# Optimization experiments

Hardware: AMD Instinct MI355X
Metric: run time of the kernel (lower is better)

## Reference

```python
import jax, jax.numpy as jnp
import numpy as np

B_SZ, SEQ, H = 8, 1024, 2048
LN_EPS = 1e-6
CLIP = 1.0e6


def setup_inputs() -> dict:
    key = jax.random.key(0)
    ks = jax.random.split(key, 8)
    lecun = 1.0 / np.sqrt(H)
    return {
        "x": jax.random.normal(ks[0], (B_SZ, SEQ, H), dtype=jnp.float32),
        "context": jnp.zeros((B_SZ, H), dtype=jnp.float32),
        # learned params
        "A": -jax.random.uniform(ks[1], (H,), dtype=jnp.float32),  # diagonal decay (zeros-init in src; small negative for stable decay)
        "Bm": jax.random.normal(ks[2], (H, H), dtype=jnp.float32) * lecun,
        "Cm": jax.random.normal(ks[3], (H, H), dtype=jnp.float32) * lecun,
        "dt_kernel": jax.random.normal(ks[4], (H, 1), dtype=jnp.float32) * 0.02,
        "dt_bias": jnp.zeros((1,), dtype=jnp.float32),
        "gate_kernel": jax.random.normal(ks[5], (H, H), dtype=jnp.float32) * lecun,
        "gate_bias": jnp.zeros((H,), dtype=jnp.float32),
        "ln_scale": jnp.ones((H,), dtype=jnp.float32),
        "ln_bias": jnp.zeros((H,), dtype=jnp.float32),
    }


def _layernorm(x, scale, bias):
    mu = jnp.mean(x, axis=-1, keepdims=True)
    var = jnp.mean(jnp.square(x - mu), axis=-1, keepdims=True)
    return (x - mu) * jax.lax.rsqrt(var + LN_EPS) * scale + bias


def reference(x, context, A, Bm, Cm, dt_kernel, dt_bias, gate_kernel, gate_bias, ln_scale, ln_bias):
    xn = jnp.clip(_layernorm(x, ln_scale, ln_bias), -CLIP, CLIP)  # [B,S,H]
    xt = jnp.swapaxes(xn, 0, 1)  # time-major [S,B,H]

    def step(state, x_t):
        # x_t: [B,H]; delta: [B,1] from Dense(1)
        delta = jnp.exp(x_t @ dt_kernel + dt_bias)
        decay = jnp.exp(delta * A)                  # [B,H] via broadcast
        new_state = state * decay + x_t @ Bm        # [B,H]
        out = new_state @ Cm                        # [B,H]
        return new_state, out

    final_state, ys = jax.lax.scan(step, context, xt)
    outputs = jnp.swapaxes(ys, 0, 1)  # [B,S,H]
    gate = outputs @ gate_kernel + gate_bias
    outputs = outputs * jax.nn.sigmoid(gate)  # GLU
    # dropout deterministic (training=False) -> identity
    return outputs, final_state
```

## Files before the change

kernel.cpp:

```cpp
#include <hip/hip_runtime.h>
#include <hip/hip_bf16.h>

#define H_DIM 2048
#define B_SZ  8
#define SEQ   1024
#define M_DIM (B_SZ*SEQ)
#define KDIM  2048
#define NKT   (KDIM/64)
#define CCH   32
#define CLEN  (SEQ/CCH)

using f32x4 = __attribute__((ext_vector_type(4))) float;
using s16x8 = __attribute__((ext_vector_type(8))) short;

__device__ __forceinline__ float bf2f(unsigned short u) {
  unsigned int x = ((unsigned int)u) << 16;
  return __builtin_bit_cast(float, x);
}
__device__ __forceinline__ unsigned short f2bf(float f) {
  unsigned int x = __builtin_bit_cast(unsigned int, f);
  unsigned int r = (x + 0x7fffu + ((x >> 16) & 1u)) >> 16;
  return (unsigned short)r;
}

__device__ __forceinline__ void gl_lds16(const void* g, void* l) {
  __builtin_amdgcn_global_load_lds(
      (__attribute__((address_space(1))) void*)g,
      (__attribute__((address_space(3))) void*)l, 16, 0, 0);
}

__global__ __launch_bounds__(256) void transpose3_kernel(
    const float* __restrict__ s0, unsigned short* __restrict__ d0,
    const float* __restrict__ s1, unsigned short* __restrict__ d1,
    const float* __restrict__ s2, unsigned short* __restrict__ d2)
{
  const float* src = (blockIdx.z == 0) ? s0 : (blockIdx.z == 1) ? s1 : s2;
  unsigned short* dst = (blockIdx.z == 0) ? d0 : (blockIdx.z == 1) ? d1 : d2;
  __shared__ float t[32][33];
  int tx = threadIdx.x & 31, ty = threadIdx.x >> 5;
  int c0 = blockIdx.x << 5, r0 = blockIdx.y << 5;
#pragma unroll
  for (int i = 0; i < 32; i += 8)
    t[ty + i][tx] = src[(size_t)(r0 + ty + i) * H_DIM + (c0 + tx)];
  __syncthreads();
#pragma unroll
  for (int i = 0; i < 32; i += 8)
    dst[(size_t)(c0 + ty + i) * H_DIM + (r0 + tx)] = f2bf(t[tx][ty + i]);
}

__global__ __launch_bounds__(256) void ln_delta_kernel(
    const float* __restrict__ x, const float* __restrict__ lns,
    const float* __restrict__ lnb, const float* __restrict__ dtk,
    const float* __restrict__ dtb, unsigned short* __restrict__ xn,
    float* __restrict__ delta)
{
  const int row = blockIdx.x;
  const int tid = threadIdx.x;
  const float* xr = x + (size_t)row * H_DIM;
  float v[8];
  *(float4*)&v[0] = ((const float4*)xr)[tid * 2];
  *(float4*)&v[4] = ((const float4*)xr)[tid * 2 + 1];
  float s1 = 0.f, s2 = 0.f;
#pragma unroll
  for (int j = 0; j < 8; ++j) { s1 += v[j]; s2 += v[j] * v[j]; }
  __shared__ float red[8];
#pragma unroll
  for (int off = 32; off; off >>= 1) {
    s1 += __shfl_down(s1, off);
    s2 += __shfl_down(s2, off);
  }
  if ((tid & 63) == 0) { red[tid >> 6] = s1; red[4 + (tid >> 6)] = s2; }
  __syncthreads();
  float mean = (red[0] + red[1] + red[2] + red[3]) * (1.0f / H_DIM);
  float var  = (red[4] + red[5] + red[6] + red[7]) * (1.0f / H_DIM) - mean * mean;
  float rstd = rsqrtf(var + 1e-6f);

  float sc[8], bi[8], dk[8];
  *(float4*)&sc[0] = ((const float4*)lns)[tid * 2];
  *(float4*)&sc[4] = ((const float4*)lns)[tid * 2 + 1];
  *(float4*)&bi[0] = ((const float4*)lnb)[tid * 2];
  *(float4*)&bi[4] = ((const float4*)lnb)[tid * 2 + 1];
  *(float4*)&dk[0] = ((const float4*)dtk)[tid * 2];
  *(float4*)&dk[4] = ((const float4*)dtk)[tid * 2 + 1];

  float dot = 0.f;
  s16x8 o;
#pragma unroll
  for (int j = 0; j < 8; ++j) {
    float xv = (v[j] - mean) * rstd * sc[j] + bi[j];
    xv = fminf(fmaxf(xv, -1.0e6f), 1.0e6f);
    dot += xv * dk[j];
    o[j] = (short)f2bf(xv);
  }
  *(s16x8*)(xn + (size_t)row * H_DIM + tid * 8) = o;

  __syncthreads();
#pragma unroll
  for (int off = 32; off; off >>= 1) dot += __shfl_down(dot, off);
  if ((tid & 63) == 0) red[tid >> 6] = dot;
  __syncthreads();
  if (tid == 0)
    delta[row] = __expf(red[0] + red[1] + red[2] + red[3] + dtb[0]);
}

__global__ __launch_bounds__(256) void scan1_kernel(
    const unsigned short* __restrict__ U, const float* __restrict__ delta,
    const float* __restrict__ Adiag, float* __restrict__ Q, float* __restrict__ P)
{
  const int h = blockIdx.x * 1024 + threadIdx.x * 4;
  const int c = blockIdx.y, b = blockIdx.z;
  const float4 a = *(const float4*)(Adiag + h);
  const unsigned short* u = U + ((size_t)b * SEQ + c * CLEN) * H_DIM + h;
  const float* dl = delta + b * SEQ + c * CLEN;
  float4 st = {0.f, 0.f, 0.f, 0.f};
  float4 pr = {1.f, 1.f, 1.f, 1.f};
#pragma unroll 8
  for (int s = 0; s < CLEN; ++s) {
    const float d = dl[s];
    const ushort4 uv = *(const ushort4*)(u + (size_t)s * H_DIM);
    const float dx = __expf(d * a.x), dy = __expf(d * a.y);
    const float dz = __expf(d * a.z), dw = __expf(d * a.w);
    st.x = fmaf(st.x, dx, bf2f(uv.x)); st.y = fmaf(st.y, dy, bf2f(uv.y));
    st.z = fmaf(st.z, dz, bf2f(uv.z)); st.w = fmaf(st.w, dw, bf2f(uv.w));
    pr.x *= dx; pr.y *= dy; pr.z *= dz; pr.w *= dw;
  }
  const size_t idx = ((size_t)b * CCH + c) * H_DIM + h;
  *(float4*)(Q + idx) = st;
  *(float4*)(P + idx) = pr;
}

__global__ __launch_bounds__(256) void scan2_kernel(
    const float* __restrict__ Q, const float* __restrict__ P,
    const float* __restrict__ ctx, float* __restrict__ sIn,
    float* __restrict__ finalSt)
{
  const int h = blockIdx.x * 256 + threadIdx.x;
  const int b = blockIdx.y;
  float s = ctx[b * H_DIM + h];
#pragma unroll
  for (int c = 0; c < CCH; ++c) {
    const size_t idx = ((size_t)b * CCH + c) * H_DIM + h;
    sIn[idx] = s;
    s = fmaf(s, P[idx], Q[idx]);
  }
  finalSt[b * H_DIM + h] = s;
}

__global__ __launch_bounds__(256) void scan3_kernel(
    const unsigned short* __restrict__ U, const float* __restrict__ delta,
    const float* __restrict__ Adiag, const float* __restrict__ sIn,
    unsigned short* __restrict__ states)
{
  const int h = blockIdx.x * 1024 + threadIdx.x * 4;
  const int c = blockIdx.y, b = blockIdx.z;
  const float4 a = *(const float4*)(Adiag + h);
  const unsigned short* u = U + ((size_t)b * SEQ + c * CLEN) * H_DIM + h;
  unsigned short* so = states + ((size_t)b * SEQ + c * CLEN) * H_DIM + h;
  const float* dl = delta + b * SEQ + c * CLEN;
  float4 st = *(const float4*)(sIn + ((size_t)b * CCH + c) * H_DIM + h);
#pragma unroll 8
  for (int s = 0; s < CLEN; ++s) {
    const float d = dl[s];
    const ushort4 uv = *(const ushort4*)(u + (size_t)s * H_DIM);
    const float dx = __expf(d * a.x), dy = __expf(d * a.y);
    const float dz = __expf(d * a.z), dw = __expf(d * a.w);
    st.x = fmaf(st.x, dx, bf2f(uv.x)); st.y = fmaf(st.y, dy, bf2f(uv.y));
    st.z = fmaf(st.z, dz, bf2f(uv.z)); st.w = fmaf(st.w, dw, bf2f(uv.w));
    ushort4 ov = { f2bf(st.x), f2bf(st.y), f2bf(st.z), f2bf(st.w) };
    *(ushort4*)(so + (size_t)s * H_DIM) = ov;
  }
}


#define BARR()  __builtin_amdgcn_s_barrier();
#define LGKM0() asm volatile("s_waitcnt lgkmcnt(0)");
#define VMC(N)  asm volatile("s_waitcnt vmcnt(" #N ")" ::: "memory");

#define RD_A(DST, PL, PHH, OFF) { _Pragma("unroll") for (int i_ = 0; i_ < 4; ++i_) { \
    DST[0][i_] = *(const s16x8*)((PL) + (OFF) + i_ * 4096); \
    DST[1][i_] = *(const s16x8*)((PHH) + (OFF) + i_ * 4096); } }
#define RD_B(DST, PL, PHH, OFF) { _Pragma("unroll") for (int j_ = 0; j_ < 2; ++j_) { \
    DST[0][j_] = *(const s16x8*)((PL) + (OFF) + j_ * 8192); \
    DST[1][j_] = *(const s16x8*)((PHH) + (OFF) + j_ * 8192); } }

#define QMM(IB, JB, AF, BF) { __builtin_amdgcn_s_setprio(1); \
  _Pragma("unroll") for (int i_ = 0; i_ < 4; ++i_) \
  _Pragma("unroll") for (int j_ = 0; j_ < 2; ++j_) { \
    acc[(IB)+i_][(JB)+j_] = __builtin_amdgcn_mfma_f32_16x16x32_bf16(AF[0][i_], BF[0][j_], acc[(IB)+i_][(JB)+j_], 0, 0, 0); \
    acc[(IB)+i_][(JB)+j_] = __builtin_amdgcn_mfma_f32_16x16x32_bf16(AF[1][i_], BF[1][j_], acc[(IB)+i_][(JB)+j_], 0, 0, 0); } \
  __builtin_amdgcn_s_setprio(0); }

#define STAGE_A(BUF, HH, TT) { const char* s_ = srcA + (HH) * 524288 + (TT) * 128; \
  char* d_ = ldsA + (BUF) * 32768 + (HH) * 16384 + tid16; \
  gl_lds16(s_, d_); gl_lds16(s_ + 262144, d_ + 8192); }
#define STAGE_B(BUF, HH, TT) { const char* s_ = srcB + (HH) * 524288 + (TT) * 128; \
  char* d_ = ldsB + (BUF) * 32768 + (HH) * 16384 + tid16; \
  gl_lds16(s_, d_); gl_lds16(s_ + 262144, d_ + 8192); }

template <int EPI>
__global__ __launch_bounds__(512, 2) void gemm8p(
    const char* __restrict__ Ab, const char* __restrict__ Bb,
    float* __restrict__ outF, unsigned short* __restrict__ outH,
    const unsigned short* __restrict__ Ybf, const float* __restrict__ gbias)
{
  extern __shared__ char lds[];
  char* ldsA = lds;
  char* ldsB = lds + 65536;

  const int tid  = threadIdx.x;
  const int lane = tid & 63, wid = tid >> 6;
  const int wr = wid >> 2, wc = wid & 3;
  const int fr = lane & 15, kq = lane >> 4;

  const int bid = blockIdx.x;
  const int xcd = bid & 7;
  const int li  = bid >> 3;
  const int bm  = (xcd >> 1) * 8 + (li & 7);
  const int bn  = (xcd & 1) * 4 + (li >> 3);

  const int grow = tid >> 3;
  const int gswz = ((tid & 7) ^ (grow & 7)) << 4;
  const char* srcA = Ab + ((size_t)(bm * 256 + grow)) * 4096 + gswz;
  const char* srcB = Bb + ((size_t)(bn * 256 + grow)) * 4096 + gswz;
  const int tid16 = tid << 4;

  const int sw0 = ((kq ^ (fr & 7)) << 4);
  const int sw1 = (((4 | kq) ^ (fr & 7)) << 4);
  const char* pa0b0 = ldsA + wr * 2048 + fr * 128 + sw0;
  const char* pa1b0 = ldsA + wr * 2048 + fr * 128 + sw1;
  const char* pa0b1 = pa0b0 + 32768;
  const char* pa1b1 = pa1b0 + 32768;
  const char* pb0b0 = ldsB + wc * 2048 + fr * 128 + sw0;
  const char* pb1b0 = ldsB + wc * 2048 + fr * 128 + sw1;
  const char* pb0b1 = pb0b0 + 32768;
  const char* pb1b1 = pb1b0 + 32768;

  f32x4 acc[8][4] = {};
  s16x8 a03[2][4], a47[2][4], b01[2][2], b23[2][2];

  STAGE_A(0, 0, 0); STAGE_B(0, 0, 0); STAGE_B(0, 1, 0); STAGE_A(0, 1, 0);
  VMC(4);
  STAGE_A(1, 0, 1); STAGE_B(1, 0, 1); STAGE_B(1, 1, 1);
  VMC(6);
  BARR();

  for (int t = 0; t < NKT / 2 - 1; ++t) {
    const int T0 = 2 * t;
    RD_A(a03, pa0b0, pa1b0, 0);
    RD_B(b01, pb0b0, pb1b0, 0);
    STAGE_A(1, 1, T0 + 1);
    BARR(); LGKM0(); QMM(0, 0, a03, b01); BARR();
    RD_B(b23, pb0b0, pb1b0, 16384);
    STAGE_A(0, 0, T0 + 2);
    BARR(); LGKM0(); QMM(0, 2, a03, b23); BARR();
    RD_A(a47, pa0b0, pa1b0, 16384);
    STAGE_B(0, 0, T0 + 2);
    BARR(); LGKM0(); QMM(4, 0, a47, b01); BARR();
    STAGE_B(0, 1, T0 + 2);
    BARR(); QMM(4, 2, a47, b23); VMC(6); BARR();
    RD_A(a03, pa0b1, pa1b1, 0);
    RD_B(b01, pb0b1, pb1b1, 0);
    STAGE_A(0, 1, T0 + 2);
    BARR(); LGKM0(); QMM(0, 0, a03, b01); BARR();
    RD_B(b23, pb0b1, pb1b1, 16384);
    STAGE_A(1, 0, T0 + 3);
    BARR(); LGKM0(); QMM(0, 2, a03, b23); BARR();
    RD_A(a47, pa0b1, pa1b1, 16384);
    STAGE_B(1, 0, T0 + 3);
    BARR(); LGKM0(); QMM(4, 0, a47, b01); BARR();
    STAGE_B(1, 1, T0 + 3);
    BARR(); QMM(4, 2, a47, b23); VMC(6); BARR();
  }

  RD_A(a03, pa0b0, pa1b0, 0);
  RD_B(b01, pb0b0, pb1b0, 0);
  STAGE_A(1, 1, 31);
  BARR(); LGKM0(); QMM(0, 0, a03, b01); BARR();
  RD_B(b23, pb0b0, pb1b0, 16384);
  BARR(); LGKM0(); QMM(0, 2, a03, b23); BARR();
  RD_A(a47, pa0b0, pa1b0, 16384);
  BARR(); LGKM0(); QMM(4, 0, a47, b01); BARR();
  BARR(); QMM(4, 2, a47, b23); VMC(0); BARR();
  RD_A(a03, pa0b1, pa1b1, 0);
  RD_B(b01, pb0b1, pb1b1, 0);
  QMM(0, 0, a03, b01);
  RD_B(b23, pb0b1, pb1b1, 16384);
  QMM(0, 2, a03, b23);
  RD_A(a47, pa0b1, pa1b1, 16384);
  QMM(4, 0, a47, b01);
  QMM(4, 2, a47, b23);

  __syncthreads();
  const int cr = (lane >> 4) << 2;
  const int cc = lane & 15;
  if constexpr (EPI == 1) {
#pragma unroll
    for (int i = 0; i < 8; ++i)
#pragma unroll
      for (int j = 0; j < 4; ++j)
#pragma unroll
        for (int r = 0; r < 4; ++r) {
          const int row = (2 * i + wr) * 16 + cr + r;
          const int col = (4 * j + wc) * 16 + cc;
          const int off = (row * 512 + col * 2) ^ ((row & 7) << 4);
          *(unsigned short*)(lds + off) = f2bf(acc[i][j][r]);
        }
    __syncthreads();
#pragma unroll
    for (int it = 0; it < 16; ++it) {
      const int L = it * 8192 + tid * 16;
      const int row = L >> 9, inrow = L & 511;
      const s16x8 v = *(const s16x8*)(lds + (L ^ ((row & 7) << 4)));
      *(s16x8*)(outH + ((size_t)(bm * 256 + row)) * H_DIM + bn * 256 + (inrow >> 1)) = v;
    }
  } else {
#pragma unroll
    for (int p = 0; p < 2; ++p) {
      if (p) __syncthreads();
#pragma unroll
      for (int i = 4 * p; i < 4 * p + 4; ++i)
#pragma unroll
        for (int j = 0; j < 4; ++j)
#pragma unroll
          for (int r = 0; r < 4; ++r) {
            const int lrow = (2 * i + wr) * 16 + cr + r - 128 * p;
            const int col = (4 * j + wc) * 16 + cc;
            const int off = (lrow * 1024 + col * 4) ^ ((lrow & 7) << 4);
            *(float*)(lds + off) = acc[i][j][r];
          }
      __syncthreads();
#pragma unroll
      for (int it = 0; it < 16; ++it) {
        const int L = it * 8192 + tid * 16;
        const int lrow = L >> 10, inrow = L & 1023;
        const f32x4 v = *(const f32x4*)(lds + (L ^ ((lrow & 7) << 4)));
        const size_t growg = (size_t)(bm * 256 + 128 * p + lrow);
        const int gcol = bn * 256 + (inrow >> 2);
        const float4 gb4 = *(const float4*)(gbias + gcol);
        const ushort4 y4 = *(const ushort4*)(Ybf + growg * H_DIM + gcol);
        float4 o;
        o.x = bf2f(y4.x) / (1.f + __expf(-(v[0] + gb4.x)));
        o.y = bf2f(y4.y) / (1.f + __expf(-(v[1] + gb4.y)));
        o.z = bf2f(y4.z) / (1.f + __expf(-(v[2] + gb4.z)));
        o.w = bf2f(y4.w) / (1.f + __expf(-(v[3] + gb4.w)));
        *(float4*)(outF + growg * H_DIM + gcol) = o;
      }
    }
  }
}

extern "C" void kernel_launch(void* const* d_in, const int* in_sizes, int n_in,
                              void* d_out, int out_size, void* d_ws, size_t ws_size,
                              hipStream_t stream) {
  (void)in_sizes; (void)n_in; (void)out_size; (void)ws_size;
  const float* x     = (const float*)d_in[0];
  const float* ctx   = (const float*)d_in[1];
  const float* Adiag = (const float*)d_in[2];
  const float* Bm    = (const float*)d_in[3];
  const float* Cm    = (const float*)d_in[4];
  const float* dtk   = (const float*)d_in[5];
  const float* dtb   = (const float*)d_in[6];
  const float* gk    = (const float*)d_in[7];
  const float* gb    = (const float*)d_in[8];
  const float* lns   = (const float*)d_in[9];
  const float* lnb   = (const float*)d_in[10];
  float* outF = (float*)d_out;

  char* ws = (char*)d_ws;
  unsigned short* xnY    = (unsigned short*)ws; ws += (size_t)M_DIM * H_DIM * 2;
  unsigned short* U      = (unsigned short*)ws; ws += (size_t)M_DIM * H_DIM * 2;
  unsigned short* states = (unsigned short*)ws; ws += (size_t)M_DIM * H_DIM * 2;
  unsigned short* T1     = (unsigned short*)ws; ws += (size_t)H_DIM * H_DIM * 2;
  unsigned short* T2     = (unsigned short*)ws; ws += (size_t)H_DIM * H_DIM * 2;
  unsigned short* T3     = (unsigned short*)ws; ws += (size_t)H_DIM * H_DIM * 2;
  float* delta           = (float*)ws;          ws += (size_t)M_DIM * 4;
  float* Qbuf            = (float*)ws;          ws += (size_t)B_SZ * CCH * H_DIM * 4;
  float* Pbuf            = (float*)ws;          ws += (size_t)B_SZ * CCH * H_DIM * 4;
  float* sInBuf          = (float*)ws;          ws += (size_t)B_SZ * CCH * H_DIM * 4;

  hipFuncSetAttribute((const void*)&gemm8p<1>,
                      hipFuncAttributeMaxDynamicSharedMemorySize, 131072);
  hipFuncSetAttribute((const void*)&gemm8p<2>,
                      hipFuncAttributeMaxDynamicSharedMemorySize, 131072);

  dim3 tb(256);
  transpose3_kernel<<<dim3(64, 64, 3), tb, 0, stream>>>(Bm, T1, Cm, T2, gk, T3);
  ln_delta_kernel<<<M_DIM, tb, 0, stream>>>(x, lns, lnb, dtk, dtb, xnY, delta);
  gemm8p<1><<<256, 512, 131072, stream>>>(
      (const char*)xnY, (const char*)T1, nullptr, U, nullptr, nullptr);
  scan1_kernel<<<dim3(H_DIM / 1024, CCH, B_SZ), tb, 0, stream>>>(
      U, delta, Adiag, Qbuf, Pbuf);
  scan2_kernel<<<dim3(H_DIM / 256, B_SZ), tb, 0, stream>>>(
      Qbuf, Pbuf, ctx, sInBuf, outF + (size_t)M_DIM * H_DIM);
  scan3_kernel<<<dim3(H_DIM / 1024, CCH, B_SZ), tb, 0, stream>>>(
      U, delta, Adiag, sInBuf, states);
  gemm8p<1><<<256, 512, 131072, stream>>>(
      (const char*)states, (const char*)T2, nullptr, xnY, nullptr, nullptr);
  gemm8p<2><<<256, 512, 131072, stream>>>(
      (const char*)xnY, (const char*)T3, outF, nullptr, xnY, gb);
}
```

Measured before the change: 252.5 us.

## Merge transpose with layernorm and fold chunk-carry scan into scan3

Combines the weight transpose/bf16 cast and the layernorm+delta kernel into one launch, dispatching on block index. Removes the separate scan2 kernel: each scan3 block now recomputes its incoming chunk state by folding the P/Q chunk summaries of all earlier chunks, and the last chunk writes the final state. This saves two kernel launches and the sIn round trip through memory. In exchange, later chunks do redundant serial work, up to 31 extra float4 loads and FMAs per thread.

Result: no change. 250.7 us (-0.7%).

```diff
diff --git a/kernel.cpp b/kernel.cpp
--- a/kernel.cpp
+++ b/kernel.cpp
@@ -29,47 +29,51 @@
       (__attribute__((address_space(3))) void*)l, 16, 0, 0);
 }
 
-__global__ __launch_bounds__(256) void transpose3_kernel(
+__global__ __launch_bounds__(256) void pre_kernel(
     const float* __restrict__ s0, unsigned short* __restrict__ d0,
     const float* __restrict__ s1, unsigned short* __restrict__ d1,
-    const float* __restrict__ s2, unsigned short* __restrict__ d2)
-{
-  const float* src = (blockIdx.z == 0) ? s0 : (blockIdx.z == 1) ? s1 : s2;
-  unsigned short* dst = (blockIdx.z == 0) ? d0 : (blockIdx.z == 1) ? d1 : d2;
-  __shared__ float t[32][33];
-  int tx = threadIdx.x & 31, ty = threadIdx.x >> 5;
-  int c0 = blockIdx.x << 5, r0 = blockIdx.y << 5;
-#pragma unroll
-  for (int i = 0; i < 32; i += 8)
-    t[ty + i][tx] = src[(size_t)(r0 + ty + i) * H_DIM + (c0 + tx)];
-  __syncthreads();
-#pragma unroll
-  for (int i = 0; i < 32; i += 8)
-    dst[(size_t)(c0 + ty + i) * H_DIM + (r0 + tx)] = f2bf(t[tx][ty + i]);
-}
-
-__global__ __launch_bounds__(256) void ln_delta_kernel(
+    const float* __restrict__ s2, unsigned short* __restrict__ d2,
     const float* __restrict__ x, const float* __restrict__ lns,
     const float* __restrict__ lnb, const float* __restrict__ dtk,
     const float* __restrict__ dtb, unsigned short* __restrict__ xn,
     float* __restrict__ delta)
 {
-  const int row = blockIdx.x;
+  __shared__ float t[32][33];
+  __shared__ float red[8];
+  const int bid = blockIdx.x;
   const int tid = threadIdx.x;
+
+  if (bid < 12288) {
+    const int z = bid >> 12;
+    const int r = bid & 4095;
+    const int c0 = (r & 63) << 5, r0 = (r >> 6) << 5;
+    const float* src = (z == 0) ? s0 : (z == 1) ? s1 : s2;
+    unsigned short* dst = (z == 0) ? d0 : (z == 1) ? d1 : d2;
+    const int tx = tid & 31, ty = tid >> 5;
+#pragma unroll
+    for (int i = 0; i < 32; i += 8)
+      t[ty + i][tx] = src[(size_t)(r0 + ty + i) * H_DIM + (c0 + tx)];
+    __syncthreads();
+#pragma unroll
+    for (int i = 0; i < 32; i += 8)
+      dst[(size_t)(c0 + ty + i) * H_DIM + (r0 + tx)] = f2bf(t[tx][ty + i]);
+    return;
+  }
+
+  const int row = bid - 12288;
   const float* xr = x + (size_t)row * H_DIM;
   float v[8];
   *(float4*)&v[0] = ((const float4*)xr)[tid * 2];
   *(float4*)&v[4] = ((const float4*)xr)[tid * 2 + 1];
-  float s1 = 0.f, s2 = 0.f;
-#pragma unroll
-  for (int j = 0; j < 8; ++j) { s1 += v[j]; s2 += v[j] * v[j]; }
-  __shared__ float red[8];
+  float sm1 = 0.f, sm2 = 0.f;
+#pragma unroll
+  for (int j = 0; j < 8; ++j) { sm1 += v[j]; sm2 += v[j] * v[j]; }
 #pragma unroll
   for (int off = 32; off; off >>= 1) {
-    s1 += __shfl_down(s1, off);
-    s2 += __shfl_down(s2, off);
-  }
-  if ((tid & 63) == 0) { red[tid >> 6] = s1; red[4 + (tid >> 6)] = s2; }
+    sm1 += __shfl_down(sm1, off);
+    sm2 += __shfl_down(sm2, off);
+  }
+  if ((tid & 63) == 0) { red[tid >> 6] = sm1; red[4 + (tid >> 6)] = sm2; }
   __syncthreads();
   float mean = (red[0] + red[1] + red[2] + red[3]) * (1.0f / H_DIM);
   float var  = (red[4] + red[5] + red[6] + red[7]) * (1.0f / H_DIM) - mean * mean;
@@ -129,35 +133,28 @@
   *(float4*)(P + idx) = pr;
 }
 
-__global__ __launch_bounds__(256) void scan2_kernel(
-    const float* __restrict__ Q, const float* __restrict__ P,
-    const float* __restrict__ ctx, float* __restrict__ sIn,
-    float* __restrict__ finalSt)
-{
-  const int h = blockIdx.x * 256 + threadIdx.x;
-  const int b = blockIdx.y;
-  float s = ctx[b * H_DIM + h];
-#pragma unroll
-  for (int c = 0; c < CCH; ++c) {
-    const size_t idx = ((size_t)b * CCH + c) * H_DIM + h;
-    sIn[idx] = s;
-    s = fmaf(s, P[idx], Q[idx]);
-  }
-  finalSt[b * H_DIM + h] = s;
-}
-
 __global__ __launch_bounds__(256) void scan3_kernel(
     const unsigned short* __restrict__ U, const float* __restrict__ delta,
-    const float* __restrict__ Adiag, const float* __restrict__ sIn,
-    unsigned short* __restrict__ states)
+    const float* __restrict__ Adiag, const float* __restrict__ Q,
+    const float* __restrict__ P, const float* __restrict__ ctx,
+    unsigned short* __restrict__ states, float* __restrict__ finalSt)
 {
   const int h = blockIdx.x * 1024 + threadIdx.x * 4;
   const int c = blockIdx.y, b = blockIdx.z;
   const float4 a = *(const float4*)(Adiag + h);
+
+  float4 st = *(const float4*)(ctx + (size_t)b * H_DIM + h);
+  for (int cc = 0; cc < c; ++cc) {
+    const size_t idx = ((size_t)b * CCH + cc) * H_DIM + h;
+    const float4 P4 = *(const float4*)(P + idx);
+    const float4 Q4 = *(const float4*)(Q + idx);
+    st.x = fmaf(st.x, P4.x, Q4.x); st.y = fmaf(st.y, P4.y, Q4.y);
+    st.z = fmaf(st.z, P4.z, Q4.z); st.w = fmaf(st.w, P4.w, Q4.w);
+  }
+
   const unsigned short* u = U + ((size_t)b * SEQ + c * CLEN) * H_DIM + h;
   unsigned short* so = states + ((size_t)b * SEQ + c * CLEN) * H_DIM + h;
   const float* dl = delta + b * SEQ + c * CLEN;
-  float4 st = *(const float4*)(sIn + ((size_t)b * CCH + c) * H_DIM + h);
 #pragma unroll 8
   for (int s = 0; s < CLEN; ++s) {
     const float d = dl[s];
@@ -169,6 +166,8 @@
     ushort4 ov = { f2bf(st.x), f2bf(st.y), f2bf(st.z), f2bf(st.w) };
     *(ushort4*)(so + (size_t)s * H_DIM) = ov;
   }
+  if (c == CCH - 1)
+    *(float4*)(finalSt + (size_t)b * H_DIM + h) = st;
 }
 
 
@@ -376,7 +375,6 @@
   float* delta           = (float*)ws;          ws += (size_t)M_DIM * 4;
   float* Qbuf            = (float*)ws;          ws += (size_t)B_SZ * CCH * H_DIM * 4;
   float* Pbuf            = (float*)ws;          ws += (size_t)B_SZ * CCH * H_DIM * 4;
-  float* sInBuf          = (float*)ws;          ws += (size_t)B_SZ * CCH * H_DIM * 4;
 
   hipFuncSetAttribute((const void*)&gemm8p<1>,
                       hipFuncAttributeMaxDynamicSharedMemorySize, 131072);
@@ -384,16 +382,14 @@
                       hipFuncAttributeMaxDynamicSharedMemorySize, 131072);
 
   dim3 tb(256);
-  transpose3_kernel<<<dim3(64, 64, 3), tb, 0, stream>>>(Bm, T1, Cm, T2, gk, T3);
-  ln_delta_kernel<<<M_DIM, tb, 0, stream>>>(x, lns, lnb, dtk, dtb, xnY, delta);
+  pre_kernel<<<12288 + M_DIM, tb, 0, stream>>>(
+      Bm, T1, Cm, T2, gk, T3, x, lns, lnb, dtk, dtb, xnY, delta);
   gemm8p<1><<<256, 512, 131072, stream>>>(
       (const char*)xnY, (const char*)T1, nullptr, U, nullptr, nullptr);
   scan1_kernel<<<dim3(H_DIM / 1024, CCH, B_SZ), tb, 0, stream>>>(
       U, delta, Adiag, Qbuf, Pbuf);
-  scan2_kernel<<<dim3(H_DIM / 256, B_SZ), tb, 0, stream>>>(
-      Qbuf, Pbuf, ctx, sInBuf, outF + (size_t)M_DIM * H_DIM);
   scan3_kernel<<<dim3(H_DIM / 1024, CCH, B_SZ), tb, 0, stream>>>(
-      U, delta, Adiag, sInBuf, states);
+      U, delta, Adiag, Qbuf, Pbuf, ctx, states, outF + (size_t)M_DIM * H_DIM);
   gemm8p<1><<<256, 512, 131072, stream>>>(
       (const char*)states, (const char*)T2, nullptr, xnY, nullptr, nullptr);
   gemm8p<2><<<256, 512, 131072, stream>>>(
```
